# Optimization experiments

Measured on AMD Instinct MI355X. Metric: run time of the kernel, lower is better.

Reference implementation:

```python
import jax, jax.numpy as jnp
import numpy as np

TOP_K = 2

def setup_inputs() -> dict:
    key = jax.random.key(0)
    ks = jax.random.split(key, 5)
    B, S, H, F, E = 2, 1024, 2048, 4096, 8
    scale_h = 1.0 / np.sqrt(H)
    scale_f = 1.0 / np.sqrt(F)
    return {
        "hidden_states": jax.random.normal(ks[0], (B, S, H), dtype=jnp.float32),
        # nn.Linear weight layout is [out, in]
        "gate_w": jax.random.normal(ks[1], (E, H), dtype=jnp.float32) * scale_h,
        "w_gate": jax.random.normal(ks[2], (E, F, H), dtype=jnp.float32) * scale_h,
        "w_up": jax.random.normal(ks[3], (E, F, H), dtype=jnp.float32) * scale_h,
        "w_down": jax.random.normal(ks[4], (E, H, F), dtype=jnp.float32) * scale_f,
    }

def reference(hidden_states, gate_w, w_gate, w_up, w_down):
    B, S, H = hidden_states.shape
    E = gate_w.shape[0]
    x = hidden_states.reshape(-1, H)                     # [T, H]
    T = x.shape[0]
    # Router: softmax -> top-k -> renormalize
    router_logits = x @ gate_w.T                         # [T, E]
    routing_weights = jax.nn.softmax(router_logits, axis=-1)
    topk_w, topk_i = jax.lax.top_k(routing_weights, TOP_K)  # [T, k]
    topk_w = topk_w / jnp.sum(topk_w, axis=-1, keepdims=True)
    # Dense [T, E] combine weights (zero for non-selected experts);
    # equivalent math to the per-expert gather/scatter loop.
    dense_w = jnp.zeros((T, E), dtype=x.dtype).at[
        jnp.arange(T)[:, None], topk_i].set(topk_w)
    # SwiGLU experts, batched over E (grouped GEMM expressed densely)
    g = jnp.einsum('th,efh->tef', x, w_gate)             # [T, E, F]
    u = jnp.einsum('th,efh->tef', x, w_up)               # [T, E, F]
    h = jax.nn.silu(g) * u                               # [T, E, F]
    y = jnp.einsum('tef,ehf->teh', h, w_down)            # [T, E, H]
    out = jnp.einsum('te,teh->th', dense_w, y)           # [T, H]
    return out.reshape(B, S, H)
```

## Files before the change

kernel.cpp:

```cpp
#include <hip/hip_runtime.h>
#include <hip/hip_bf16.h>


#define T_TOK 2048
#define H_DIM 2048
#define F_DIM 4096
#define E_NUM 8
#define NPAIR (T_TOK * 2)

typedef __attribute__((ext_vector_type(8))) short short8;
typedef __attribute__((ext_vector_type(4))) float f32x4;

__device__ __forceinline__ unsigned short f2bf(float f) {
    unsigned u = __builtin_bit_cast(unsigned, f);
    u = (u + 0x7FFFu + ((u >> 16) & 1u)) >> 16;
    return (unsigned short)u;
}

__device__ __forceinline__ uint4 pack8(float4 a, float4 b) {
    uint4 o;
    o.x = f2bf(a.x) | ((unsigned)f2bf(a.y) << 16);
    o.y = f2bf(a.z) | ((unsigned)f2bf(a.w) << 16);
    o.z = f2bf(b.x) | ((unsigned)f2bf(b.y) << 16);
    o.w = f2bf(b.z) | ((unsigned)f2bf(b.w) << 16);
    return o;
}

__device__ __forceinline__ uint2 pack4(float4 a) {
    uint2 o;
    o.x = f2bf(a.x) | ((unsigned)f2bf(a.y) << 16);
    o.y = f2bf(a.z) | ((unsigned)f2bf(a.w) << 16);
    return o;
}

__device__ __forceinline__ void gload16(const void* g, void* s) {
    __builtin_amdgcn_global_load_lds(
        (const __attribute__((address_space(1))) unsigned int*)g,
        (__attribute__((address_space(3))) unsigned int*)s, 16, 0, 0);
}

__global__ void k_cvt_x(const float* __restrict__ x, ushort* __restrict__ xb) {
    int i = blockIdx.x * blockDim.x + threadIdx.x;
    const float4* p = (const float4*)x + (size_t)i * 2;
    uint2 lo = pack4(p[0]), hi = pack4(p[1]);
    ((uint4*)xb)[i] = make_uint4(lo.x, lo.y, hi.x, hi.y);
}

__global__ void k_router(const float* __restrict__ x, const float* __restrict__ gw,
                         int2* __restrict__ eidx, float2* __restrict__ ew,
                         int* __restrict__ cnt) {
    int t = blockIdx.x * 4 + (threadIdx.x >> 6);
    int lane = threadIdx.x & 63;
    const float* xr = x + (size_t)t * H_DIM;
    float l[E_NUM];
    #pragma unroll
    for (int e = 0; e < E_NUM; e++) {
        const float* wr = gw + (size_t)e * H_DIM;
        float acc = 0.f;
        for (int i = lane; i < H_DIM; i += 64) acc += xr[i] * wr[i];
        #pragma unroll
        for (int o = 32; o; o >>= 1) acc += __shfl_xor(acc, o);
        l[e] = acc;
    }
    if (lane == 0) {
        int e0 = 0;
        #pragma unroll
        for (int e = 1; e < E_NUM; e++) if (l[e] > l[e0]) e0 = e;
        int e1 = -1;
        #pragma unroll
        for (int e = 0; e < E_NUM; e++) {
            if (e == e0) continue;
            if (e1 < 0 || l[e] > l[e1]) e1 = e;
        }
        float s1 = expf(l[e1] - l[e0]);
        float w0 = 1.f / (1.f + s1);
        float w1 = s1 * w0;
        eidx[t] = make_int2(e0, e1);
        ew[t]   = make_float2(w0, w1);
        atomicAdd(&cnt[e0], 1);
        atomicAdd(&cnt[e1], 1);
    }
}

__global__ void k_off(const int* __restrict__ cnt, int* __restrict__ off,
                      int* __restrict__ cnt2) {
    if (threadIdx.x == 0) {
        int s = 0;
        for (int e = 0; e < E_NUM; e++) { off[e] = s; s += cnt[e]; cnt2[e] = 0; }
        off[E_NUM] = s;
    }
}

__global__ void k_fill(const int2* __restrict__ eidx, const float2* __restrict__ ew,
                       const int* __restrict__ off, int* __restrict__ cnt2,
                       int* __restrict__ ptok, int2* __restrict__ inv) {
    int t = blockIdx.x * blockDim.x + threadIdx.x;
    if (t >= T_TOK) return;
    int2 e = eidx[t];
    int p0 = off[e.x] + atomicAdd(&cnt2[e.x], 1);
    ptok[p0] = t;
    int p1 = off[e.y] + atomicAdd(&cnt2[e.y], 1);
    ptok[p1] = t;
    inv[t] = make_int2(p0, p1);
}

__global__ __launch_bounds__(512, 4) void k_gemm1(
        const ushort* __restrict__ xb, const float* __restrict__ wg,
        const float* __restrict__ wu, const int* __restrict__ ptok,
        const int* __restrict__ off, ushort* __restrict__ hbuf) {
    __shared__ __align__(16) ushort As[256 * 64];
    __shared__ __align__(16) ushort Bg[64 * 64];
    __shared__ __align__(16) ushort Bu[64 * 64];

    int e = blockIdx.y >> 4, mt = blockIdx.y & 15;
    int base = off[e], ne = off[e + 1] - base;
    int row0 = mt * 256;
    if (row0 >= ne) return;
    int nb = blockIdx.x * 64;

    int tid = threadIdx.x;
    int wv = tid >> 6, l = tid & 63;
    int lr = l & 15, lk = l >> 4;
    int wm = wv >> 1, wn = wv & 1;

    int wvu = __builtin_amdgcn_readfirstlane(wv);
    const ushort* srcA[4];
    int sslot = 8 * ((l & 7) ^ ((l >> 3) & 7));
    #pragma unroll
    for (int c = 0; c < 4; c++) {
        int r = (wvu * 4 + c) * 8 + (l >> 3);
        int pp = base + min(row0 + r, ne - 1);
        srcA[c] = xb + (size_t)ptok[pp] * H_DIM + sslot;
    }

    int brow = tid >> 3, bs = tid & 7;
    const float* wgrow = wg + ((size_t)e * F_DIM + nb + brow) * H_DIM + bs * 8;
    const float* wurow = wu + ((size_t)e * F_DIM + nb + brow) * H_DIM + bs * 8;
    int bo = brow * 64 + (((bs * 16) ^ ((brow & 7) << 4)) >> 1);

    int rsw = (lr & 7) << 4;

    f32x4 accg[4][2] = {}; f32x4 accu[4][2] = {};

    for (int kb = 0; kb < H_DIM; kb += 64) {
        __syncthreads();
        #pragma unroll
        for (int c = 0; c < 4; c++)
            gload16(srcA[c] + kb, (ushort*)As + (wvu * 4 + c) * 512);
        float4 g0 = *(const float4*)(wgrow + kb);
        float4 g1 = *(const float4*)(wgrow + kb + 4);
        *(uint4*)(&Bg[bo]) = pack8(g0, g1);
        float4 u0 = *(const float4*)(wurow + kb);
        float4 u1 = *(const float4*)(wurow + kb + 4);
        *(uint4*)(&Bu[bo]) = pack8(u0, u1);
        __syncthreads();

        #pragma unroll
        for (int kk = 0; kk < 2; kk++) {
            int kby = kk * 64 + lk * 16;
            short8 a[4];
            #pragma unroll
            for (int m = 0; m < 4; m++) {
                int row = wm * 64 + m * 16 + lr;
                a[m] = *(const short8*)(&As[(row * 128 + (kby ^ rsw)) >> 1]);
            }
            #pragma unroll
            for (int n = 0; n < 2; n++) {
                int rowb = wn * 32 + n * 16 + lr;
                int boff = (rowb * 128 + (kby ^ rsw)) >> 1;
                short8 bg8 = *(const short8*)(&Bg[boff]);
                short8 bu8 = *(const short8*)(&Bu[boff]);
                #pragma unroll
                for (int m = 0; m < 4; m++) {
                    accg[m][n] = __builtin_amdgcn_mfma_f32_16x16x32_bf16(a[m], bg8, accg[m][n], 0, 0, 0);
                    accu[m][n] = __builtin_amdgcn_mfma_f32_16x16x32_bf16(a[m], bu8, accu[m][n], 0, 0, 0);
                }
            }
        }
    }

    #pragma unroll
    for (int m = 0; m < 4; m++) {
        #pragma unroll
        for (int r = 0; r < 4; r++) {
            int lrow = wm * 64 + m * 16 + lk * 4 + r;
            if (row0 + lrow < ne) {
                size_t rb = (size_t)(base + row0 + lrow) * F_DIM + nb;
                #pragma unroll
                for (int n = 0; n < 2; n++) {
                    float g = accg[m][n][r], u = accu[m][n][r];
                    float hv = g / (1.f + __expf(-g)) * u;
                    hbuf[rb + wn * 32 + n * 16 + lr] = f2bf(hv);
                }
            }
        }
    }
}

__global__ __launch_bounds__(512, 2) void k_gemm2(
        const ushort* __restrict__ hbuf, const float* __restrict__ wd,
        const int* __restrict__ off, float* __restrict__ ybuf) {
    __shared__ __align__(16) ushort As[256 * 64];
    __shared__ __align__(16) ushort Bs[128 * 64];

    int e = blockIdx.y >> 3, mt = blockIdx.y & 7;
    int base = off[e], ne = off[e + 1] - base;
    int row0 = mt * 256;
    if (row0 >= ne) return;
    int nb = blockIdx.x * 128;

    int tid = threadIdx.x;
    int wv = tid >> 6, l = tid & 63;
    int lr = l & 15, lk = l >> 4;
    int wm = wv >> 1, wn = wv & 1;

    int wvu = __builtin_amdgcn_readfirstlane(wv);
    const ushort* srcA[4];
    int sslot = 8 * ((l & 7) ^ ((l >> 3) & 7));
    #pragma unroll
    for (int c = 0; c < 4; c++) {
        int r = (wvu * 4 + c) * 8 + (l >> 3);
        int pp = base + min(row0 + r, ne - 1);
        srcA[c] = hbuf + (size_t)pp * F_DIM + sslot;
    }

    int brow = tid >> 2, bs = tid & 3;
    const float* wdrow = wd + ((size_t)e * H_DIM + nb + brow) * F_DIM + bs * 16;
    int bsw = (brow & 7) << 4;
    int bo0 = brow * 64 + (((bs * 32) ^ bsw) >> 1);
    int bo1 = brow * 64 + (((bs * 32 + 16) ^ bsw) >> 1);

    int rsw = (lr & 7) << 4;

    f32x4 acc[4][4] = {};

    for (int kb = 0; kb < F_DIM; kb += 64) {
        __syncthreads();
        #pragma unroll
        for (int c = 0; c < 4; c++)
            gload16(srcA[c] + kb, (ushort*)As + (wvu * 4 + c) * 512);
        float4 b0 = *(const float4*)(wdrow + kb);
        float4 b1 = *(const float4*)(wdrow + kb + 4);
        float4 b2 = *(const float4*)(wdrow + kb + 8);
        float4 b3 = *(const float4*)(wdrow + kb + 12);
        *(uint4*)(&Bs[bo0]) = pack8(b0, b1);
        *(uint4*)(&Bs[bo1]) = pack8(b2, b3);
        __syncthreads();

        #pragma unroll
        for (int kk = 0; kk < 2; kk++) {
            int kby = kk * 64 + lk * 16;
            short8 a[4];
            #pragma unroll
            for (int m = 0; m < 4; m++) {
                int row = wm * 64 + m * 16 + lr;
                a[m] = *(const short8*)(&As[(row * 128 + (kby ^ rsw)) >> 1]);
            }
            #pragma unroll
            for (int n = 0; n < 4; n++) {
                int rowb = wn * 64 + n * 16 + lr;
                short8 b8 = *(const short8*)(&Bs[(rowb * 128 + (kby ^ rsw)) >> 1]);
                #pragma unroll
                for (int m = 0; m < 4; m++)
                    acc[m][n] = __builtin_amdgcn_mfma_f32_16x16x32_bf16(a[m], b8, acc[m][n], 0, 0, 0);
            }
        }
    }

    #pragma unroll
    for (int m = 0; m < 4; m++) {
        #pragma unroll
        for (int r = 0; r < 4; r++) {
            int lrow = wm * 64 + m * 16 + lk * 4 + r;
            if (row0 + lrow < ne) {
                float* yrow = ybuf + (size_t)(base + row0 + lrow) * H_DIM + nb;
                #pragma unroll
                for (int n = 0; n < 4; n++)
                    yrow[wn * 64 + n * 16 + lr] = acc[m][n][r];
            }
        }
    }
}

__global__ void k_combine(const float* __restrict__ ybuf,
                          const float2* __restrict__ ew,
                          const int2* __restrict__ inv,
                          float* __restrict__ out) {
    int t = blockIdx.x;
    float2 w = ew[t];
    int2 pp = inv[t];
    const float4* y0 = (const float4*)(ybuf + (size_t)pp.x * H_DIM);
    const float4* y1 = (const float4*)(ybuf + (size_t)pp.y * H_DIM);
    float4* o = (float4*)(out + (size_t)t * H_DIM);
    for (int j = threadIdx.x; j < H_DIM / 4; j += blockDim.x) {
        float4 a = y0[j], b = y1[j];
        float4 r;
        r.x = w.x * a.x + w.y * b.x;
        r.y = w.x * a.y + w.y * b.y;
        r.z = w.x * a.z + w.y * b.z;
        r.w = w.x * a.w + w.y * b.w;
        o[j] = r;
    }
}

extern "C" void kernel_launch(void* const* d_in, const int* in_sizes, int n_in,
                              void* d_out, int out_size, void* d_ws, size_t ws_size,
                              hipStream_t stream) {
    const float* x  = (const float*)d_in[0];
    const float* gw = (const float*)d_in[1];
    const float* wg = (const float*)d_in[2];
    const float* wu = (const float*)d_in[3];
    const float* wd = (const float*)d_in[4];
    float* out = (float*)d_out;

    char* ws = (char*)d_ws;
    size_t o = 0;
    ushort* xb   = (ushort*)(ws + o); o += (size_t)T_TOK * H_DIM * 2;
    ushort* hbuf = (ushort*)(ws + o); o += (size_t)NPAIR * F_DIM * 2;
    float*  ybuf = (float*) (ws + o); o += (size_t)NPAIR * H_DIM * 4;
    int*    ptok = (int*)   (ws + o); o += NPAIR * 4;
    int2*   eidx = (int2*)  (ws + o); o += T_TOK * 8;
    float2* ew   = (float2*)(ws + o); o += T_TOK * 8;
    int2*   inv  = (int2*)  (ws + o); o += T_TOK * 8;
    int*    cnt  = (int*)   (ws + o); o += 256;
    int*    cnt2 = (int*)   (ws + o); o += 256;
    int*    off  = (int*)   (ws + o); o += 256;

    hipMemsetAsync(cnt, 0, 256, stream);

    k_cvt_x <<<T_TOK * H_DIM / 8 / 256, 256, 0, stream>>>(x, xb);
    k_router<<<T_TOK / 4, 256, 0, stream>>>(x, gw, eidx, ew, cnt);
    k_off   <<<1, 64, 0, stream>>>(cnt, off, cnt2);
    k_fill  <<<T_TOK / 256, 256, 0, stream>>>(eidx, ew, off, cnt2, ptok, inv);

    dim3 g1(F_DIM / 64, E_NUM * 16);
    k_gemm1<<<g1, 512, 0, stream>>>(xb, wg, wu, ptok, off, hbuf);
    dim3 g2(H_DIM / 128, E_NUM * 8);
    k_gemm2<<<g2, 512, 0, stream>>>(hbuf, wd, off, ybuf);
    k_combine<<<T_TOK, 256, 0, stream>>>(ybuf, ew, inv, out);
}
```

Measured before the change: 575.3 us.

## Pre-convert down-projection weights to bf16 inside gemm1 and use direct-load gemm2

Extra blocks are appended to the gemm1 grid that convert the fp32 w_down weights to a bf16 workspace copy, running alongside the gate/up GEMM. A new gemm2 variant then streams bf16 weights straight into LDS with the same 16-byte load path used for activations, instead of reading fp32 and converting per tile. The gemm1 M-tile grid is also halved, since 8 tiles of 256 rows already cover the largest possible expert. The goal is to cut gemm2's weight bandwidth and conversion work. The cost is an extra 128MB workspace write plus a fixed 128-block conversion that may form a tail in gemm1. A fallback to the fp32 path is kept when the workspace is too small.

```diff
diff --git a/kernel.cpp b/kernel.cpp
--- a/kernel.cpp
+++ b/kernel.cpp
@@ -107,12 +107,24 @@
 __global__ __launch_bounds__(512, 4) void k_gemm1(
         const ushort* __restrict__ xb, const float* __restrict__ wg,
         const float* __restrict__ wu, const int* __restrict__ ptok,
-        const int* __restrict__ off, ushort* __restrict__ hbuf) {
+        const int* __restrict__ off, ushort* __restrict__ hbuf,
+        const float* __restrict__ wd, ushort* __restrict__ wdb) {
     __shared__ __align__(16) ushort As[256 * 64];
     __shared__ __align__(16) ushort Bg[64 * 64];
     __shared__ __align__(16) ushort Bu[64 * 64];
 
-    int e = blockIdx.y >> 4, mt = blockIdx.y & 15;
+    if (blockIdx.x >= F_DIM / 64) {
+        int worker = (blockIdx.x - F_DIM / 64) * 64 + blockIdx.y;
+        const size_t total8 = (size_t)E_NUM * H_DIM * F_DIM / 8;
+        for (size_t i = (size_t)worker * 512 + threadIdx.x; i < total8;
+             i += (size_t)128 * 512) {
+            const float4* p = (const float4*)wd + i * 2;
+            ((uint4*)wdb)[i] = pack8(p[0], p[1]);
+        }
+        return;
+    }
+
+    int e = blockIdx.y >> 3, mt = blockIdx.y & 7;
     int base = off[e], ne = off[e + 1] - base;
     int row0 = mt * 256;
     if (row0 >= ne) return;
@@ -197,7 +209,89 @@
     }
 }
 
-__global__ __launch_bounds__(512, 2) void k_gemm2(
+__global__ __launch_bounds__(512, 2) void k_gemm2b(
+        const ushort* __restrict__ hbuf, const ushort* __restrict__ wdb,
+        const int* __restrict__ off, float* __restrict__ ybuf) {
+    __shared__ __align__(16) ushort As[256 * 64];
+    __shared__ __align__(16) ushort Bs[128 * 64];
+
+    int e = blockIdx.y >> 3, mt = blockIdx.y & 7;
+    int base = off[e], ne = off[e + 1] - base;
+    int row0 = mt * 256;
+    if (row0 >= ne) return;
+    int nb = blockIdx.x * 128;
+
+    int tid = threadIdx.x;
+    int wv = tid >> 6, l = tid & 63;
+    int lr = l & 15, lk = l >> 4;
+    int wm = wv >> 1, wn = wv & 1;
+
+    int wvu = __builtin_amdgcn_readfirstlane(wv);
+    int sslot = 8 * ((l & 7) ^ ((l >> 3) & 7));
+    const ushort* srcA[4];
+    #pragma unroll
+    for (int c = 0; c < 4; c++) {
+        int r = (wvu * 4 + c) * 8 + (l >> 3);
+        int pp = base + min(row0 + r, ne - 1);
+        srcA[c] = hbuf + (size_t)pp * F_DIM + sslot;
+    }
+    const ushort* srcB[2];
+    #pragma unroll
+    for (int c = 0; c < 2; c++) {
+        int r = wvu * 16 + c * 8 + (l >> 3);
+        srcB[c] = wdb + ((size_t)e * H_DIM + nb + r) * F_DIM + sslot;
+    }
+
+    int rsw = (lr & 7) << 4;
+
+    f32x4 acc[4][4] = {};
+
+    for (int kb = 0; kb < F_DIM; kb += 64) {
+        __syncthreads();
+        #pragma unroll
+        for (int c = 0; c < 4; c++)
+            gload16(srcA[c] + kb, (ushort*)As + (wvu * 4 + c) * 512);
+        #pragma unroll
+        for (int c = 0; c < 2; c++)
+            gload16(srcB[c] + kb, (ushort*)Bs + (wvu * 2 + c) * 512);
+        __syncthreads();
+
+        #pragma unroll
+        for (int kk = 0; kk < 2; kk++) {
+            int kby = kk * 64 + lk * 16;
+            short8 a[4];
+            #pragma unroll
+            for (int m = 0; m < 4; m++) {
+                int row = wm * 64 + m * 16 + lr;
+                a[m] = *(const short8*)(&As[(row * 128 + (kby ^ rsw)) >> 1]);
+            }
+            #pragma unroll
+            for (int n = 0; n < 4; n++) {
+                int rowb = wn * 64 + n * 16 + lr;
+                short8 b8 = *(const short8*)(&Bs[(rowb * 128 + (kby ^ rsw)) >> 1]);
+                #pragma unroll
+                for (int m = 0; m < 4; m++)
+                    acc[m][n] = __builtin_amdgcn_mfma_f32_16x16x32_bf16(a[m], b8, acc[m][n], 0, 0, 0);
+            }
+        }
+    }
+
+    #pragma unroll
+    for (int m = 0; m < 4; m++) {
+        #pragma unroll
+        for (int r = 0; r < 4; r++) {
+            int lrow = wm * 64 + m * 16 + lk * 4 + r;
+            if (row0 + lrow < ne) {
+                float* yrow = ybuf + (size_t)(base + row0 + lrow) * H_DIM + nb;
+                #pragma unroll
+                for (int n = 0; n < 4; n++)
+                    yrow[wn * 64 + n * 16 + lr] = acc[m][n][r];
+            }
+        }
+    }
+}
+
+__global__ __launch_bounds__(512, 2) void k_gemm2f(
         const ushort* __restrict__ hbuf, const float* __restrict__ wd,
         const int* __restrict__ off, float* __restrict__ ybuf) {
     __shared__ __align__(16) ushort As[256 * 64];
@@ -325,6 +419,8 @@
     int*    cnt  = (int*)   (ws + o); o += 256;
     int*    cnt2 = (int*)   (ws + o); o += 256;
     int*    off  = (int*)   (ws + o); o += 256;
+    ushort* wdb  = (ushort*)(ws + o); o += (size_t)E_NUM * H_DIM * F_DIM * 2;
+    bool bf16w = (ws_size >= o);
 
     hipMemsetAsync(cnt, 0, 256, stream);
 
@@ -333,9 +429,16 @@
     k_off   <<<1, 64, 0, stream>>>(cnt, off, cnt2);
     k_fill  <<<T_TOK / 256, 256, 0, stream>>>(eidx, ew, off, cnt2, ptok, inv);
 
-    dim3 g1(F_DIM / 64, E_NUM * 16);
-    k_gemm1<<<g1, 512, 0, stream>>>(xb, wg, wu, ptok, off, hbuf);
-    dim3 g2(H_DIM / 128, E_NUM * 8);
-    k_gemm2<<<g2, 512, 0, stream>>>(hbuf, wd, off, ybuf);
+    if (bf16w) {
+        dim3 g1(F_DIM / 64 + 2, E_NUM * 8);
+        k_gemm1<<<g1, 512, 0, stream>>>(xb, wg, wu, ptok, off, hbuf, wd, wdb);
+        dim3 g2(H_DIM / 128, E_NUM * 8);
+        k_gemm2b<<<g2, 512, 0, stream>>>(hbuf, wdb, off, ybuf);
+    } else {
+        dim3 g1(F_DIM / 64, E_NUM * 8);
+        k_gemm1<<<g1, 512, 0, stream>>>(xb, wg, wu, ptok, off, hbuf, wd, wdb);
+        dim3 g2(H_DIM / 128, E_NUM * 8);
+        k_gemm2f<<<g2, 512, 0, stream>>>(hbuf, wd, off, ybuf);
+    }
     k_combine<<<T_TOK, 256, 0, stream>>>(ybuf, ew, inv, out);
 }
```

Measured after the change: 640.9 us. 11.4% more time.

## Prefetch expert weight tiles into registers one K-step ahead in both GEMMs

Applied to the files above, without the earlier changes.

Both expert GEMM loops now issue the fp32 weight loads for the next K tile right after the shared-memory barrier. They keep those values in registers, so global-load latency overlaps the MFMA work of the current tile instead of stalling before the LDS store. The MFMA section is wrapped in s_setprio to favour the compute waves. The gemm1 launch bound drops from 4 to 3 blocks per CU to leave room for the extra live registers. The gemm1 grid is also halved to 8 M-tiles per expert, which still covers the 2048-row maximum and removes blocks that only returned early. The cost is higher register pressure and possibly lower occupancy.

```diff
diff --git a/kernel.cpp b/kernel.cpp
--- a/kernel.cpp
+++ b/kernel.cpp
@@ -104,7 +104,7 @@
     inv[t] = make_int2(p0, p1);
 }
 
-__global__ __launch_bounds__(512, 4) void k_gemm1(
+__global__ __launch_bounds__(512, 3) void k_gemm1(
         const ushort* __restrict__ xb, const float* __restrict__ wg,
         const float* __restrict__ wu, const int* __restrict__ ptok,
         const int* __restrict__ off, ushort* __restrict__ hbuf) {
@@ -112,7 +112,7 @@
     __shared__ __align__(16) ushort Bg[64 * 64];
     __shared__ __align__(16) ushort Bu[64 * 64];
 
-    int e = blockIdx.y >> 4, mt = blockIdx.y & 15;
+    int e = blockIdx.y >> 3, mt = blockIdx.y & 7;
     int base = off[e], ne = off[e + 1] - base;
     int row0 = mt * 256;
     if (row0 >= ne) return;
@@ -142,19 +142,29 @@
 
     f32x4 accg[4][2] = {}; f32x4 accu[4][2] = {};
 
-    for (int kb = 0; kb < H_DIM; kb += 64) {
+    float4 pg0 = *(const float4*)(wgrow);
+    float4 pg1 = *(const float4*)(wgrow + 4);
+    float4 pu0 = *(const float4*)(wurow);
+    float4 pu1 = *(const float4*)(wurow + 4);
+
+    const int NT = H_DIM / 64;
+    for (int kt = 0; kt < NT; kt++) {
+        int kb = kt * 64;
         __syncthreads();
         #pragma unroll
         for (int c = 0; c < 4; c++)
             gload16(srcA[c] + kb, (ushort*)As + (wvu * 4 + c) * 512);
-        float4 g0 = *(const float4*)(wgrow + kb);
-        float4 g1 = *(const float4*)(wgrow + kb + 4);
-        *(uint4*)(&Bg[bo]) = pack8(g0, g1);
-        float4 u0 = *(const float4*)(wurow + kb);
-        float4 u1 = *(const float4*)(wurow + kb + 4);
-        *(uint4*)(&Bu[bo]) = pack8(u0, u1);
+        *(uint4*)(&Bg[bo]) = pack8(pg0, pg1);
+        *(uint4*)(&Bu[bo]) = pack8(pu0, pu1);
         __syncthreads();
-
+        if (kt + 1 < NT) {
+            int kn = kb + 64;
+            pg0 = *(const float4*)(wgrow + kn);
+            pg1 = *(const float4*)(wgrow + kn + 4);
+            pu0 = *(const float4*)(wurow + kn);
+            pu1 = *(const float4*)(wurow + kn + 4);
+        }
+        __builtin_amdgcn_s_setprio(1);
         #pragma unroll
         for (int kk = 0; kk < 2; kk++) {
             int kby = kk * 64 + lk * 16;
@@ -177,6 +187,7 @@
                 }
             }
         }
+        __builtin_amdgcn_s_setprio(0);
     }
 
     #pragma unroll
@@ -234,19 +245,29 @@
 
     f32x4 acc[4][4] = {};
 
-    for (int kb = 0; kb < F_DIM; kb += 64) {
+    float4 pb0 = *(const float4*)(wdrow);
+    float4 pb1 = *(const float4*)(wdrow + 4);
+    float4 pb2 = *(const float4*)(wdrow + 8);
+    float4 pb3 = *(const float4*)(wdrow + 12);
+
+    const int NT = F_DIM / 64;
+    for (int kt = 0; kt < NT; kt++) {
+        int kb = kt * 64;
         __syncthreads();
         #pragma unroll
         for (int c = 0; c < 4; c++)
             gload16(srcA[c] + kb, (ushort*)As + (wvu * 4 + c) * 512);
-        float4 b0 = *(const float4*)(wdrow + kb);
-        float4 b1 = *(const float4*)(wdrow + kb + 4);
-        float4 b2 = *(const float4*)(wdrow + kb + 8);
-        float4 b3 = *(const float4*)(wdrow + kb + 12);
-        *(uint4*)(&Bs[bo0]) = pack8(b0, b1);
-        *(uint4*)(&Bs[bo1]) = pack8(b2, b3);
+        *(uint4*)(&Bs[bo0]) = pack8(pb0, pb1);
+        *(uint4*)(&Bs[bo1]) = pack8(pb2, pb3);
         __syncthreads();
-
+        if (kt + 1 < NT) {
+            int kn = kb + 64;
+            pb0 = *(const float4*)(wdrow + kn);
+            pb1 = *(const float4*)(wdrow + kn + 4);
+            pb2 = *(const float4*)(wdrow + kn + 8);
+            pb3 = *(const float4*)(wdrow + kn + 12);
+        }
+        __builtin_amdgcn_s_setprio(1);
         #pragma unroll
         for (int kk = 0; kk < 2; kk++) {
             int kby = kk * 64 + lk * 16;
@@ -265,6 +286,7 @@
                     acc[m][n] = __builtin_amdgcn_mfma_f32_16x16x32_bf16(a[m], b8, acc[m][n], 0, 0, 0);
             }
         }
+        __builtin_amdgcn_s_setprio(0);
     }
 
     #pragma unroll
@@ -333,7 +355,7 @@
     k_off   <<<1, 64, 0, stream>>>(cnt, off, cnt2);
     k_fill  <<<T_TOK / 256, 256, 0, stream>>>(eidx, ew, off, cnt2, ptok, inv);
 
-    dim3 g1(F_DIM / 64, E_NUM * 16);
+    dim3 g1(F_DIM / 64, E_NUM * 8);
     k_gemm1<<<g1, 512, 0, stream>>>(xb, wg, wu, ptok, off, hbuf);
     dim3 g2(H_DIM / 128, E_NUM * 8);
     k_gemm2<<<g2, 512, 0, stream>>>(hbuf, wd, off, ybuf);
```

Result: slower. 648.2 us (+12.7%).
